# Kernel tuning notes

Measured on AMD Instinct MI355X. Metric: run time of the kernel, lower is better.

Reference implementation:

```python
import jax, jax.numpy as jnp
import numpy as np

THETA = 10000.0


def rope_apply(x, pos, theta=THETA):
    # x: [..., S, d] with d even; rotates interleaved pairs (2k, 2k+1),
    # matching the block-diag 2x2 rotation matmul in the torch RoPE.
    d = x.shape[-1]
    half = d // 2
    inv_freq = 1.0 / (theta ** (2.0 * jnp.arange(half, dtype=jnp.float32) / d))
    ang = pos.astype(jnp.float32)[:, None] * inv_freq[None, :]  # [S, half]
    cos, sin = jnp.cos(ang), jnp.sin(ang)
    xe, xo = x[..., 0::2], x[..., 1::2]
    oe = cos * xe - sin * xo
    oo = sin * xe + cos * xo
    return jnp.stack([oe, oo], axis=-1).reshape(x.shape)


def setup_inputs() -> dict:
    key = jax.random.key(0)
    ks = jax.random.split(key, 5)
    B, S, D = 2, 2048, 1024
    scale = 0.02
    return {
        "x": jax.random.normal(ks[0], (B, S, D), dtype=jnp.float32),
        "token_positions": jnp.arange(S, dtype=jnp.int64 if jax.config.jax_enable_x64 else jnp.int32),
        "wq": jax.random.normal(ks[1], (D, D), dtype=jnp.float32) * scale,
        "wk": jax.random.normal(ks[2], (D, D), dtype=jnp.float32) * scale,
        "wv": jax.random.normal(ks[3], (D, D), dtype=jnp.float32) * scale,
        "wo": jax.random.normal(ks[4], (D, D), dtype=jnp.float32) * scale,
    }


def reference(x, token_positions, wq, wk, wv, wo):
    B, S, D = x.shape
    H = 16
    dk = D // H

    def split_heads(t):  # [B,S,D] -> [B,H,S,dk]
        return t.reshape(B, S, H, dk).swapaxes(1, 2)

    q = split_heads(jnp.einsum('bsd,ed->bse', x, wq))
    k = split_heads(jnp.einsum('bsd,ed->bse', x, wk))
    v = split_heads(jnp.einsum('bsd,ed->bse', x, wv))

    q = rope_apply(q, token_positions)
    k = rope_apply(k, token_positions)

    scores = jnp.einsum('bhqd,bhkd->bhqk', q, k) / jnp.sqrt(jnp.float32(dk))
    causal = jnp.tril(jnp.ones((S, S), dtype=bool))
    scores = jnp.where(causal, scores, -jnp.inf)
    p = jax.nn.softmax(scores, axis=-1)
    o = jnp.einsum('bhqk,bhkd->bhqd', p, v)          # [B,H,S,dk]
    o = o.swapaxes(1, 2).reshape(B, S, D)            # merge heads
    return jnp.einsum('bse,de->bsd', o, wo)          # out proj (wo.T)
```

## Files before the change

### kernel.cpp

```cpp
#include <hip/hip_runtime.h>

typedef unsigned short u16;
typedef __attribute__((ext_vector_type(8))) short short8;
typedef __attribute__((ext_vector_type(4))) float f32x4;

__device__ __forceinline__ u16 f2b(float f) {
  union { float f; unsigned u; } v; v.f = f;
  unsigned u = v.u;
  return (u16)((u + 0x7FFFu + ((u >> 16) & 1u)) >> 16);
}
__device__ __forceinline__ u16 f2b_trunc(float f) {
  union { float f; unsigned u; } v; v.f = f;
  return (u16)(v.u >> 16);
}
__device__ __forceinline__ void glds16(const u16* g, u16* l) {
  __builtin_amdgcn_global_load_lds((const __attribute__((address_space(1))) void*)g,
                                   (__attribute__((address_space(3))) void*)l, 16, 0, 0);
}

__global__ __launch_bounds__(256) void prep_k(const float* __restrict__ x,
                                              const float* __restrict__ wq,
                                              const float* __restrict__ wk,
                                              const float* __restrict__ wv,
                                              const float* __restrict__ wo,
                                              const int* __restrict__ pos,
                                              u16* __restrict__ xb,
                                              u16* __restrict__ wqkvb,
                                              u16* __restrict__ wob,
                                              float* __restrict__ cs) {
  int bx = blockIdx.x, tid = threadIdx.x;
  if (bx < 8192) {
    const float* src; u16* dst; int base;
    if (bx < 4096)      { src = x;  dst = xb;                base = bx; }
    else if (bx < 5120) { src = wq; dst = wqkvb;             base = bx - 4096; }
    else if (bx < 6144) { src = wk; dst = wqkvb + (1 << 20); base = bx - 5120; }
    else if (bx < 7168) { src = wv; dst = wqkvb + (2 << 20); base = bx - 6144; }
    else                { src = wo; dst = wob;               base = bx - 7168; }
    int i4 = base * 1024 + tid * 4;
    const float4 v = *(const float4*)(src + i4);
    uint2 o;
    o.x = (unsigned)f2b(v.x) | ((unsigned)f2b(v.y) << 16);
    o.y = (unsigned)f2b(v.z) | ((unsigned)f2b(v.w) << 16);
    *(uint2*)(dst + i4) = o;
  } else {
    int idx = (bx - 8192) * 256 + tid;
    int i = idx & 31, s = idx >> 5;
    float p = (float)pos[s];
    float inv = expf(-(float)i * (logf(10000.0f) / 32.0f));
    float ang = p * inv;
    cs[idx * 2]     = cosf(ang);
    cs[idx * 2 + 1] = sinf(ang);
  }
}

__global__ __launch_bounds__(128, 3) void gemm_qkv(const u16* __restrict__ A,
                                                   const u16* __restrict__ B,
                                                   const float* __restrict__ cs,
                                                   u16* __restrict__ Qr,
                                                   u16* __restrict__ Kr,
                                                   u16* __restrict__ VTg) {
  const int K = 1024;
  __shared__ u16 As[64 * 64];
  __shared__ u16 Bs[128 * 64];
  const int tid = threadIdx.x;
  const int wv = tid >> 6, lane = tid & 63;
  const int quad = lane >> 4, l16 = lane & 15;
  const int m0 = blockIdx.y * 64, n0 = blockIdx.x * 128;
  const int sw = l16 & 7;

  f32x4 acc[4][4];
  for (int i = 0; i < 4; i++)
    for (int j = 0; j < 4; j++) acc[i][j] = (f32x4){0.f, 0.f, 0.f, 0.f};

  for (int kt = 0; kt < K; kt += 64) {
    __syncthreads();
#pragma unroll
    for (int p = 0; p < 4; p++) {
      int c = p * 128 + tid;
      int row = c >> 3, k8 = (c & 7) ^ (row & 7);
      glds16(A + (size_t)(m0 + row) * K + kt + k8 * 8, As + (size_t)(c & ~63) * 8);
    }
#pragma unroll
    for (int p = 0; p < 8; p++) {
      int c = p * 128 + tid;
      int row = c >> 3, k8 = (c & 7) ^ (row & 7);
      glds16(B + (size_t)(n0 + row) * K + kt + k8 * 8, Bs + (size_t)(c & ~63) * 8);
    }
    __syncthreads();
#pragma unroll
    for (int half = 0; half < 2; half++) {
      short8 af[4], bfr[4];
      const int kc = ((half * 4 + quad) ^ sw) * 8;
#pragma unroll
      for (int i = 0; i < 4; i++)
        af[i] = *(const short8*)(As + (i * 16 + l16) * 64 + kc);
#pragma unroll
      for (int j = 0; j < 4; j++)
        bfr[j] = *(const short8*)(Bs + (wv * 64 + j * 16 + l16) * 64 + kc);
#pragma unroll
      for (int i = 0; i < 4; i++)
#pragma unroll
        for (int j = 0; j < 4; j++)
          acc[i][j] = __builtin_amdgcn_mfma_f32_16x16x32_bf16(af[i], bfr[j], acc[i][j], 0, 0, 0);
    }
  }

  const int region = n0 >> 10;
  const int b = m0 >> 11;
  if (region < 2) {
    u16* dst = region ? Kr : Qr;
    const bool evn = (l16 & 1) == 0;
    for (int i = 0; i < 4; i++)
      for (int j = 0; j < 4; j++) {
        int col = n0 + wv * 64 + j * 16 + l16;
        int cq = col & 1023;
        int h = cq >> 6, d = cq & 63, ifr = (d >> 1) & 31;
        for (int r = 0; r < 4; r++) {
          int s = (m0 & 2047) + i * 16 + quad * 4 + r;
          float v = acc[i][j][r];
          float vp = __shfl_xor(v, 1);
          if (evn) {
            float2 c2 = *(const float2*)(cs + (s * 32 + ifr) * 2);
            float oe = c2.x * v - c2.y * vp;
            float oo = c2.y * v + c2.x * vp;
            unsigned pk = (unsigned)f2b(oe) | ((unsigned)f2b(oo) << 16);
            *(unsigned*)(dst + ((size_t)(b * 16 + h) * 2048 + s) * 64 + d) = pk;
          }
        }
      }
  } else {
    for (int j = 0; j < 4; j++) {
      int col = n0 + wv * 64 + j * 16 + l16;
      int cq = col & 1023;
      int h = cq >> 6, d = cq & 63;
      u16* base = VTg + ((size_t)(b * 16 + h) * 64 + d) * 2048;
      for (int i = 0; i < 4; i++) {
        int s0 = (m0 & 2047) + i * 16 + quad * 4;
        uint2 o;
        o.x = (unsigned)f2b(acc[i][j][0]) | ((unsigned)f2b(acc[i][j][1]) << 16);
        o.y = (unsigned)f2b(acc[i][j][2]) | ((unsigned)f2b(acc[i][j][3]) << 16);
        *(uint2*)(base + s0) = o;
      }
    }
  }
}

__global__ __launch_bounds__(128, 3) void gemm_bt_f32(const u16* __restrict__ A,
                                                      const u16* __restrict__ B,
                                                      float* __restrict__ C,
                                                      int M, int N, int K) {
  __shared__ u16 As[64 * 64];
  __shared__ u16 Bs[128 * 64];
  const int tid = threadIdx.x;
  const int wv = tid >> 6, lane = tid & 63;
  const int quad = lane >> 4, l16 = lane & 15;
  const int m0 = blockIdx.y * 64, n0 = blockIdx.x * 128;
  const int sw = l16 & 7;

  f32x4 acc[4][4];
  for (int i = 0; i < 4; i++)
    for (int j = 0; j < 4; j++) acc[i][j] = (f32x4){0.f, 0.f, 0.f, 0.f};

  for (int kt = 0; kt < K; kt += 64) {
    __syncthreads();
#pragma unroll
    for (int p = 0; p < 4; p++) {
      int c = p * 128 + tid;
      int row = c >> 3, k8 = (c & 7) ^ (row & 7);
      glds16(A + (size_t)(m0 + row) * K + kt + k8 * 8, As + (size_t)(c & ~63) * 8);
    }
#pragma unroll
    for (int p = 0; p < 8; p++) {
      int c = p * 128 + tid;
      int row = c >> 3, k8 = (c & 7) ^ (row & 7);
      glds16(B + (size_t)(n0 + row) * K + kt + k8 * 8, Bs + (size_t)(c & ~63) * 8);
    }
    __syncthreads();
#pragma unroll
    for (int half = 0; half < 2; half++) {
      short8 af[4], bfr[4];
      const int kc = ((half * 4 + quad) ^ sw) * 8;
#pragma unroll
      for (int i = 0; i < 4; i++)
        af[i] = *(const short8*)(As + (i * 16 + l16) * 64 + kc);
#pragma unroll
      for (int j = 0; j < 4; j++)
        bfr[j] = *(const short8*)(Bs + (wv * 64 + j * 16 + l16) * 64 + kc);
#pragma unroll
      for (int i = 0; i < 4; i++)
#pragma unroll
        for (int j = 0; j < 4; j++)
          acc[i][j] = __builtin_amdgcn_mfma_f32_16x16x32_bf16(af[i], bfr[j], acc[i][j], 0, 0, 0);
    }
  }
  for (int i = 0; i < 4; i++)
    for (int j = 0; j < 4; j++) {
      int col = n0 + wv * 64 + j * 16 + l16;
      for (int r = 0; r < 4; r++) {
        int row = m0 + i * 16 + quad * 4 + r;
        C[(size_t)row * N + col] = acc[i][j][r];
      }
    }
}

__global__ __launch_bounds__(256, 6) void attn_k(const u16* __restrict__ Q,
                                                 const u16* __restrict__ K,
                                                 const u16* __restrict__ VT,
                                                 u16* __restrict__ O, int S) {
  __shared__ u16 Ks[8 * 512], Vt[64 * 64], Ps[8 * 520];
  const int tid = threadIdx.x;
  const int wv = tid >> 6, lane = tid & 63, quad = lane >> 4, l16 = lane & 15;
  const int bh = blockIdx.x;
  const int yy = blockIdx.y, k4 = yy >> 3, g = yy & 7;
  const int qt = (k4 & 1) ? (k4 * 8 + 7 - g) : (k4 * 8 + g);
  const int q0 = qt * 64;
  const u16* Qg = Q + (size_t)bh * S * 64;
  const u16* Kg = K + (size_t)bh * S * 64;
  const u16* Vg = VT + (size_t)bh * S * 64;
  const float scale2 = 0.125f * 1.44269504f;
  const int rowbase = wv * 16 + quad * 4;

  const int vrow_off = lane >> 3;
  const int vchunk = (lane & 7) ^ (lane >> 3);

  const u16* qrow = Qg + (size_t)(q0 + wv * 16 + l16) * 64;
  short8 qa0 = *(const short8*)(qrow + quad * 8);
  short8 qa1 = *(const short8*)(qrow + 32 + quad * 8);

  f32x4 oacc[4];
  for (int j = 0; j < 4; j++) oacc[j] = (f32x4){0.f, 0.f, 0.f, 0.f};
  float l_r[4] = {0.f, 0.f, 0.f, 0.f};

  for (int kt = 0; kt <= qt; kt++) {
    const int k0 = kt * 64;
    __syncthreads();
    for (int p = wv; p < 8; p += 4) {
      glds16(Kg + (size_t)(k0 + lane) * 64 + p * 8, Ks + p * 512);
      glds16(Vg + (size_t)(p * 8 + vrow_off) * S + k0 + vchunk * 8, Vt + p * 512);
    }
    __syncthreads();

    const bool diag = (kt == qt);
#pragma unroll
    for (int nt = 0; nt < 4; nt++) {
      f32x4 s4 = (f32x4){0.f, 0.f, 0.f, 0.f};
      short8 b0 = *(const short8*)(Ks + quad * 512 + (nt * 16 + l16) * 8);
      short8 b1 = *(const short8*)(Ks + (4 + quad) * 512 + (nt * 16 + l16) * 8);
      s4 = __builtin_amdgcn_mfma_f32_16x16x32_bf16(qa0, b0, s4, 0, 0, 0);
      s4 = __builtin_amdgcn_mfma_f32_16x16x32_bf16(qa1, b1, s4, 0, 0, 0);
      int col = nt * 16 + l16;
      int cp = col >> 3, co = col & 7;
      if (!diag) {
#pragma unroll
        for (int r = 0; r < 4; r++) {
          float v = fminf(s4[r] * scale2, 86.f);
          float p = exp2f(v);
          l_r[r] += p;
          int row = rowbase + r;
          int A = (cp + 2 * (row >> 3)) & 7;
          Ps[A * 520 + row * 8 + co] = f2b_trunc(p);
        }
      } else {
#pragma unroll
        for (int r = 0; r < 4; r++) {
          float v = fminf(s4[r] * scale2, 86.f);
          if (col > rowbase + r) v = -1e30f;
          float p = exp2f(v);
          l_r[r] += p;
          int row = rowbase + r;
          int A = (cp + 2 * (row >> 3)) & 7;
          Ps[A * 520 + row * 8 + co] = f2b_trunc(p);
        }
      }
    }
    {
      int mr = wv * 16 + l16;
      int A0 = (quad + 2 * (mr >> 3)) & 7;
      short8 pa0 = *(const short8*)(Ps + A0 * 520 + mr * 8);
      short8 pa1 = *(const short8*)(Ps + ((A0 + 4) & 7) * 520 + mr * 8);
      int sl0 = quad ^ (l16 & 7);
#pragma unroll
      for (int nt = 0; nt < 4; nt++) {
        int d = nt * 16 + l16;
        short8 vb0 = *(const short8*)(Vt + d * 64 + sl0 * 8);
        short8 vb1 = *(const short8*)(Vt + d * 64 + (sl0 ^ 4) * 8);
        oacc[nt] = __builtin_amdgcn_mfma_f32_16x16x32_bf16(pa0, vb0, oacc[nt], 0, 0, 0);
        oacc[nt] = __builtin_amdgcn_mfma_f32_16x16x32_bf16(pa1, vb1, oacc[nt], 0, 0, 0);
      }
    }
  }
#pragma unroll
  for (int r = 0; r < 4; r++) {
    l_r[r] += __shfl_xor(l_r[r], 1);
    l_r[r] += __shfl_xor(l_r[r], 2);
    l_r[r] += __shfl_xor(l_r[r], 4);
    l_r[r] += __shfl_xor(l_r[r], 8);
    l_r[r] = 1.f / l_r[r];
  }
  const int b = bh >> 4, h = bh & 15;
  const bool evn = (l16 & 1) == 0;
#pragma unroll
  for (int nt = 0; nt < 4; nt++) {
    int col = nt * 16 + l16;
#pragma unroll
    for (int r = 0; r < 4; r++) {
      float v = oacc[nt][r] * l_r[r];
      float vp = __shfl_xor(v, 1);
      if (evn) {
        int s = q0 + rowbase + r;
        unsigned pk = (unsigned)f2b(v) | ((unsigned)f2b(vp) << 16);
        *(unsigned*)(O + ((size_t)(b * S + s) * 16 + h) * 64 + col) = pk;
      }
    }
  }
}

extern "C" void kernel_launch(void* const* d_in, const int* in_sizes, int n_in,
                              void* d_out, int out_size, void* d_ws, size_t ws_size,
                              hipStream_t stream) {
  const float* x  = (const float*)d_in[0];
  const int*   tp = (const int*)d_in[1];
  const float* wq = (const float*)d_in[2];
  const float* wk = (const float*)d_in[3];
  const float* wvp = (const float*)d_in[4];
  const float* wo = (const float*)d_in[5];
  float* out = (float*)d_out;

  const int S = 2048, D = 1024;
  const int BS = 2 * S;

  char* ws = (char*)d_ws;
  u16*   xb    = (u16*)(ws);
  u16*   wqkvb = (u16*)(ws + ((size_t)8 << 20));
  u16*   wob   = (u16*)(ws + ((size_t)14 << 20));
  float* cs    = (float*)(ws + ((size_t)16 << 20));
  u16*   qr    = (u16*)(ws + ((size_t)17 << 20));
  u16*   kr    = (u16*)(ws + ((size_t)25 << 20));
  u16*   vtg   = (u16*)(ws + ((size_t)33 << 20));
  u16*   ob    = (u16*)(ws + ((size_t)42 << 20));

  prep_k<<<8448, 256, 0, stream>>>(x, wq, wk, wvp, wo, tp, xb, wqkvb, wob, cs);

  dim3 g1(3 * D / 128, BS / 64);
  gemm_qkv<<<g1, 128, 0, stream>>>(xb, wqkvb, cs, qr, kr, vtg);

  dim3 ga(32, 32);
  attn_k<<<ga, 256, 0, stream>>>(qr, kr, vtg, ob, S);

  dim3 g2(D / 128, BS / 64);
  gemm_bt_f32<<<g2, 128, 0, stream>>>(ob, wob, out, BS, D, D);
}
```

Measured before the change: 205.1 us.

## Pair causal query tiles per block and double-buffer K/V loads

Each attention block now handles two query tiles, slot and 31-slot, so causal work is balanced across blocks and every K/V tile loaded into shared memory serves both tiles. K/V tiles are double-buffered so the load of the next tile overlaps compute on the current one, which removes one barrier per iteration. The grid is halved to 512 blocks and launch bounds drop from 6 to 2 blocks per CU. This raises register and LDS use and lowers occupancy.

```diff
diff --git a/kernel.cpp b/kernel.cpp
--- a/kernel.cpp
+++ b/kernel.cpp
@@ -203,113 +203,123 @@
     }
 }
 
-__global__ __launch_bounds__(256, 6) void attn_k(const u16* __restrict__ Q,
+__global__ __launch_bounds__(256, 2) void attn_k(const u16* __restrict__ Q,
                                                  const u16* __restrict__ K,
                                                  const u16* __restrict__ VT,
                                                  u16* __restrict__ O, int S) {
-  __shared__ u16 Ks[8 * 512], Vt[64 * 64], Ps[8 * 520];
+  __shared__ u16 Ks[2][8 * 512], Vt[2][8 * 512];
+  __shared__ u16 PsA[8 * 520], PsB[8 * 520];
   const int tid = threadIdx.x;
   const int wv = tid >> 6, lane = tid & 63, quad = lane >> 4, l16 = lane & 15;
-  const int bh = blockIdx.x;
-  const int yy = blockIdx.y, k4 = yy >> 3, g = yy & 7;
-  const int qt = (k4 & 1) ? (k4 * 8 + 7 - g) : (k4 * 8 + g);
-  const int q0 = qt * 64;
+  const int bh = blockIdx.x, slot = blockIdx.y;
+  const int qtA = slot, qtB = 31 - slot;
+  const int q0A = qtA * 64, q0B = qtB * 64;
   const u16* Qg = Q + (size_t)bh * S * 64;
   const u16* Kg = K + (size_t)bh * S * 64;
   const u16* Vg = VT + (size_t)bh * S * 64;
   const float scale2 = 0.125f * 1.44269504f;
   const int rowbase = wv * 16 + quad * 4;
-
   const int vrow_off = lane >> 3;
   const int vchunk = (lane & 7) ^ (lane >> 3);
 
-  const u16* qrow = Qg + (size_t)(q0 + wv * 16 + l16) * 64;
-  short8 qa0 = *(const short8*)(qrow + quad * 8);
-  short8 qa1 = *(const short8*)(qrow + 32 + quad * 8);
-
-  f32x4 oacc[4];
-  for (int j = 0; j < 4; j++) oacc[j] = (f32x4){0.f, 0.f, 0.f, 0.f};
-  float l_r[4] = {0.f, 0.f, 0.f, 0.f};
-
-  for (int kt = 0; kt <= qt; kt++) {
-    const int k0 = kt * 64;
-    __syncthreads();
-    for (int p = wv; p < 8; p += 4) {
-      glds16(Kg + (size_t)(k0 + lane) * 64 + p * 8, Ks + p * 512);
-      glds16(Vg + (size_t)(p * 8 + vrow_off) * S + k0 + vchunk * 8, Vt + p * 512);
-    }
-    __syncthreads();
-
-    const bool diag = (kt == qt);
+  const u16* qrowA = Qg + (size_t)(q0A + wv * 16 + l16) * 64;
+  short8 qa0A = *(const short8*)(qrowA + quad * 8);
+  short8 qa1A = *(const short8*)(qrowA + 32 + quad * 8);
+  const u16* qrowB = Qg + (size_t)(q0B + wv * 16 + l16) * 64;
+  short8 qa0B = *(const short8*)(qrowB + quad * 8);
+  short8 qa1B = *(const short8*)(qrowB + 32 + quad * 8);
+
+  f32x4 oaccA[4], oaccB[4];
+  for (int j = 0; j < 4; j++) {
+    oaccA[j] = (f32x4){0.f, 0.f, 0.f, 0.f};
+    oaccB[j] = (f32x4){0.f, 0.f, 0.f, 0.f};
+  }
+  float lA[4] = {0.f, 0.f, 0.f, 0.f}, lB[4] = {0.f, 0.f, 0.f, 0.f};
+
+  auto compute = [&](short8 qa0, short8 qa1, const u16* Ksb, const u16* Vtb,
+                     u16* Psb, f32x4* oacc, float* l_r, bool diag) {
 #pragma unroll
     for (int nt = 0; nt < 4; nt++) {
       f32x4 s4 = (f32x4){0.f, 0.f, 0.f, 0.f};
-      short8 b0 = *(const short8*)(Ks + quad * 512 + (nt * 16 + l16) * 8);
-      short8 b1 = *(const short8*)(Ks + (4 + quad) * 512 + (nt * 16 + l16) * 8);
+      short8 b0 = *(const short8*)(Ksb + quad * 512 + (nt * 16 + l16) * 8);
+      short8 b1 = *(const short8*)(Ksb + (4 + quad) * 512 + (nt * 16 + l16) * 8);
       s4 = __builtin_amdgcn_mfma_f32_16x16x32_bf16(qa0, b0, s4, 0, 0, 0);
       s4 = __builtin_amdgcn_mfma_f32_16x16x32_bf16(qa1, b1, s4, 0, 0, 0);
       int col = nt * 16 + l16;
       int cp = col >> 3, co = col & 7;
-      if (!diag) {
-#pragma unroll
-        for (int r = 0; r < 4; r++) {
-          float v = fminf(s4[r] * scale2, 86.f);
-          float p = exp2f(v);
-          l_r[r] += p;
-          int row = rowbase + r;
-          int A = (cp + 2 * (row >> 3)) & 7;
-          Ps[A * 520 + row * 8 + co] = f2b_trunc(p);
-        }
-      } else {
-#pragma unroll
-        for (int r = 0; r < 4; r++) {
-          float v = fminf(s4[r] * scale2, 86.f);
-          if (col > rowbase + r) v = -1e30f;
-          float p = exp2f(v);
-          l_r[r] += p;
-          int row = rowbase + r;
-          int A = (cp + 2 * (row >> 3)) & 7;
-          Ps[A * 520 + row * 8 + co] = f2b_trunc(p);
-        }
-      }
-    }
-    {
-      int mr = wv * 16 + l16;
-      int A0 = (quad + 2 * (mr >> 3)) & 7;
-      short8 pa0 = *(const short8*)(Ps + A0 * 520 + mr * 8);
-      short8 pa1 = *(const short8*)(Ps + ((A0 + 4) & 7) * 520 + mr * 8);
-      int sl0 = quad ^ (l16 & 7);
-#pragma unroll
-      for (int nt = 0; nt < 4; nt++) {
-        int d = nt * 16 + l16;
-        short8 vb0 = *(const short8*)(Vt + d * 64 + sl0 * 8);
-        short8 vb1 = *(const short8*)(Vt + d * 64 + (sl0 ^ 4) * 8);
-        oacc[nt] = __builtin_amdgcn_mfma_f32_16x16x32_bf16(pa0, vb0, oacc[nt], 0, 0, 0);
-        oacc[nt] = __builtin_amdgcn_mfma_f32_16x16x32_bf16(pa1, vb1, oacc[nt], 0, 0, 0);
-      }
-    }
-  }
-#pragma unroll
-  for (int r = 0; r < 4; r++) {
-    l_r[r] += __shfl_xor(l_r[r], 1);
-    l_r[r] += __shfl_xor(l_r[r], 2);
-    l_r[r] += __shfl_xor(l_r[r], 4);
-    l_r[r] += __shfl_xor(l_r[r], 8);
-    l_r[r] = 1.f / l_r[r];
-  }
+#pragma unroll
+      for (int r = 0; r < 4; r++) {
+        float v = fminf(s4[r] * scale2, 86.f);
+        if (diag && col > rowbase + r) v = -1e30f;
+        float p = exp2f(v);
+        l_r[r] += p;
+        int row = rowbase + r;
+        int A = (cp + 2 * (row >> 3)) & 7;
+        Psb[A * 520 + row * 8 + co] = f2b_trunc(p);
+      }
+    }
+    int mr = wv * 16 + l16;
+    int A0 = (quad + 2 * (mr >> 3)) & 7;
+    short8 pa0 = *(const short8*)(Psb + A0 * 520 + mr * 8);
+    short8 pa1 = *(const short8*)(Psb + ((A0 + 4) & 7) * 520 + mr * 8);
+    int sl0 = quad ^ (l16 & 7);
+#pragma unroll
+    for (int nt = 0; nt < 4; nt++) {
+      int d = nt * 16 + l16;
+      short8 vb0 = *(const short8*)(Vtb + d * 64 + sl0 * 8);
+      short8 vb1 = *(const short8*)(Vtb + d * 64 + (sl0 ^ 4) * 8);
+      oacc[nt] = __builtin_amdgcn_mfma_f32_16x16x32_bf16(pa0, vb0, oacc[nt], 0, 0, 0);
+      oacc[nt] = __builtin_amdgcn_mfma_f32_16x16x32_bf16(pa1, vb1, oacc[nt], 0, 0, 0);
+    }
+  };
+
+  for (int p = wv; p < 8; p += 4) {
+    glds16(Kg + (size_t)(lane)*64 + p * 8, &Ks[0][p * 512]);
+    glds16(Vg + (size_t)(p * 8 + vrow_off) * S + vchunk * 8, &Vt[0][p * 512]);
+  }
+
+  for (int kt = 0; kt <= qtB; kt++) {
+    const int cur = kt & 1;
+    __syncthreads();
+    if (kt < qtB) {
+      const int kn = (kt + 1) * 64;
+      for (int p = wv; p < 8; p += 4) {
+        glds16(Kg + (size_t)(kn + lane) * 64 + p * 8, &Ks[cur ^ 1][p * 512]);
+        glds16(Vg + (size_t)(p * 8 + vrow_off) * S + kn + vchunk * 8, &Vt[cur ^ 1][p * 512]);
+      }
+    }
+    compute(qa0B, qa1B, &Ks[cur][0], &Vt[cur][0], PsB, oaccB, lB, kt == qtB);
+    if (kt <= qtA)
+      compute(qa0A, qa1A, &Ks[cur][0], &Vt[cur][0], PsA, oaccA, lA, kt == qtA);
+  }
+
   const int b = bh >> 4, h = bh & 15;
   const bool evn = (l16 & 1) == 0;
 #pragma unroll
+  for (int r = 0; r < 4; r++) {
+    lA[r] += __shfl_xor(lA[r], 1); lA[r] += __shfl_xor(lA[r], 2);
+    lA[r] += __shfl_xor(lA[r], 4); lA[r] += __shfl_xor(lA[r], 8);
+    lA[r] = 1.f / lA[r];
+    lB[r] += __shfl_xor(lB[r], 1); lB[r] += __shfl_xor(lB[r], 2);
+    lB[r] += __shfl_xor(lB[r], 4); lB[r] += __shfl_xor(lB[r], 8);
+    lB[r] = 1.f / lB[r];
+  }
+#pragma unroll
   for (int nt = 0; nt < 4; nt++) {
     int col = nt * 16 + l16;
 #pragma unroll
     for (int r = 0; r < 4; r++) {
-      float v = oacc[nt][r] * l_r[r];
-      float vp = __shfl_xor(v, 1);
+      float vA = oaccA[nt][r] * lA[r];
+      float vAp = __shfl_xor(vA, 1);
+      float vB = oaccB[nt][r] * lB[r];
+      float vBp = __shfl_xor(vB, 1);
       if (evn) {
-        int s = q0 + rowbase + r;
-        unsigned pk = (unsigned)f2b(v) | ((unsigned)f2b(vp) << 16);
-        *(unsigned*)(O + ((size_t)(b * S + s) * 16 + h) * 64 + col) = pk;
+        int sA = q0A + rowbase + r;
+        unsigned pkA = (unsigned)f2b(vA) | ((unsigned)f2b(vAp) << 16);
+        *(unsigned*)(O + ((size_t)(b * S + sA) * 16 + h) * 64 + col) = pkA;
+        int sB = q0B + rowbase + r;
+        unsigned pkB = (unsigned)f2b(vB) | ((unsigned)f2b(vBp) << 16);
+        *(unsigned*)(O + ((size_t)(b * S + sB) * 16 + h) * 64 + col) = pkB;
       }
     }
   }
@@ -344,7 +354,7 @@
   dim3 g1(3 * D / 128, BS / 64);
   gemm_qkv<<<g1, 128, 0, stream>>>(xb, wqkvb, cs, qr, kr, vtg);
 
-  dim3 ga(32, 32);
+  dim3 ga(32, 16);
   attn_k<<<ga, 256, 0, stream>>>(qr, kr, vtg, ob, S);
 
   dim3 g2(D / 128, BS / 64);
```

New measurement: 198.0 us. 1.04x faster.

## Pair complementary causal query tiles per block, double-buffer K/V, prescale Q

Applied to the files above, without the earlier changes.

Each attention block now has 512 threads in two wave groups. One group handles query tile `slot` and the other handles tile 31-slot, so every block does the same amount of causal work while sharing the K/V tiles it stages. K/V loads into LDS are double-buffered so the next tile's global-to-LDS copy is issued before the current tile is computed. The softmax scale and log2e factor are folded into Q in the QKV GEMM epilogue, which removes a multiply and the clamp from the inner loop; dropping the fminf clamp slightly changes overflow safety. The grid halves and LDS use per block grows, which changes occupancy.

```diff
diff --git a/kernel.cpp b/kernel.cpp
--- a/kernel.cpp
+++ b/kernel.cpp
@@ -109,6 +109,7 @@
   const int b = m0 >> 11;
   if (region < 2) {
     u16* dst = region ? Kr : Qr;
+    const float qs = region ? 1.0f : 0.125f * 1.44269504f;
     const bool evn = (l16 & 1) == 0;
     for (int i = 0; i < 4; i++)
       for (int j = 0; j < 4; j++) {
@@ -121,8 +122,8 @@
           float vp = __shfl_xor(v, 1);
           if (evn) {
             float2 c2 = *(const float2*)(cs + (s * 32 + ifr) * 2);
-            float oe = c2.x * v - c2.y * vp;
-            float oo = c2.y * v + c2.x * vp;
+            float oe = (c2.x * v - c2.y * vp) * qs;
+            float oo = (c2.y * v + c2.x * vp) * qs;
             unsigned pk = (unsigned)f2b(oe) | ((unsigned)f2b(oo) << 16);
             *(unsigned*)(dst + ((size_t)(b * 16 + h) * 2048 + s) * 64 + d) = pk;
           }
@@ -203,102 +204,105 @@
     }
 }
 
-__global__ __launch_bounds__(256, 6) void attn_k(const u16* __restrict__ Q,
+struct AttnSM {
+  u16 Ks[2][8 * 512];
+  u16 Vt[2][8 * 512];
+  u16 Ps[2][8 * 520];
+};
+
+template <bool DIAG>
+__device__ __forceinline__ void attn_tile(const u16* Ksb, const u16* Vtb, u16* Psb,
+                                          short8 qa0, short8 qa1, f32x4* oacc,
+                                          float* l_r, int wl, int quad, int l16) {
+  const int rowbase = wl * 16 + quad * 4;
+#pragma unroll
+  for (int nt = 0; nt < 4; nt++) {
+    f32x4 s4 = (f32x4){0.f, 0.f, 0.f, 0.f};
+    short8 b0 = *(const short8*)(Ksb + quad * 512 + (nt * 16 + l16) * 8);
+    short8 b1 = *(const short8*)(Ksb + (4 + quad) * 512 + (nt * 16 + l16) * 8);
+    s4 = __builtin_amdgcn_mfma_f32_16x16x32_bf16(qa0, b0, s4, 0, 0, 0);
+    s4 = __builtin_amdgcn_mfma_f32_16x16x32_bf16(qa1, b1, s4, 0, 0, 0);
+    int col = nt * 16 + l16;
+    int cp = col >> 3, co = col & 7;
+#pragma unroll
+    for (int r = 0; r < 4; r++) {
+      float v = s4[r];
+      if (DIAG && col > rowbase + r) v = -1e30f;
+      float p = exp2f(v);
+      l_r[r] += p;
+      int row = rowbase + r;
+      int A = (cp + 2 * (row >> 3)) & 7;
+      Psb[A * 520 + row * 8 + co] = f2b_trunc(p);
+    }
+  }
+  int mr = wl * 16 + l16;
+  int A0 = (quad + 2 * (mr >> 3)) & 7;
+  short8 pa0 = *(const short8*)(Psb + A0 * 520 + mr * 8);
+  short8 pa1 = *(const short8*)(Psb + ((A0 + 4) & 7) * 520 + mr * 8);
+  int sl0 = quad ^ (l16 & 7);
+#pragma unroll
+  for (int nt = 0; nt < 4; nt++) {
+    int d = nt * 16 + l16;
+    short8 vb0 = *(const short8*)(Vtb + d * 64 + sl0 * 8);
+    short8 vb1 = *(const short8*)(Vtb + d * 64 + (sl0 ^ 4) * 8);
+    oacc[nt] = __builtin_amdgcn_mfma_f32_16x16x32_bf16(pa0, vb0, oacc[nt], 0, 0, 0);
+    oacc[nt] = __builtin_amdgcn_mfma_f32_16x16x32_bf16(pa1, vb1, oacc[nt], 0, 0, 0);
+  }
+}
+
+__global__ __launch_bounds__(512, 4) void attn_k(const u16* __restrict__ Q,
                                                  const u16* __restrict__ K,
                                                  const u16* __restrict__ VT,
                                                  u16* __restrict__ O, int S) {
-  __shared__ u16 Ks[8 * 512], Vt[64 * 64], Ps[8 * 520];
+  __shared__ AttnSM sm;
   const int tid = threadIdx.x;
   const int wv = tid >> 6, lane = tid & 63, quad = lane >> 4, l16 = lane & 15;
-  const int bh = blockIdx.x;
-  const int yy = blockIdx.y, k4 = yy >> 3, g = yy & 7;
-  const int qt = (k4 & 1) ? (k4 * 8 + 7 - g) : (k4 * 8 + g);
-  const int q0 = qt * 64;
+  const int grp = wv >> 2, wl = wv & 3;
+  const int bh = blockIdx.x, slot = blockIdx.y;
+  const int qtB = 31 - slot;
+  const int qtMy = grp ? qtB : slot;
+  const int q0My = qtMy * 64;
   const u16* Qg = Q + (size_t)bh * S * 64;
   const u16* Kg = K + (size_t)bh * S * 64;
   const u16* Vg = VT + (size_t)bh * S * 64;
-  const float scale2 = 0.125f * 1.44269504f;
-  const int rowbase = wv * 16 + quad * 4;
-
   const int vrow_off = lane >> 3;
   const int vchunk = (lane & 7) ^ (lane >> 3);
 
-  const u16* qrow = Qg + (size_t)(q0 + wv * 16 + l16) * 64;
+  const u16* qrow = Qg + (size_t)(q0My + wl * 16 + l16) * 64;
   short8 qa0 = *(const short8*)(qrow + quad * 8);
   short8 qa1 = *(const short8*)(qrow + 32 + quad * 8);
 
   f32x4 oacc[4];
   for (int j = 0; j < 4; j++) oacc[j] = (f32x4){0.f, 0.f, 0.f, 0.f};
   float l_r[4] = {0.f, 0.f, 0.f, 0.f};
-
-  for (int kt = 0; kt <= qt; kt++) {
-    const int k0 = kt * 64;
-    __syncthreads();
-    for (int p = wv; p < 8; p += 4) {
-      glds16(Kg + (size_t)(k0 + lane) * 64 + p * 8, Ks + p * 512);
-      glds16(Vg + (size_t)(p * 8 + vrow_off) * S + k0 + vchunk * 8, Vt + p * 512);
-    }
-    __syncthreads();
-
-    const bool diag = (kt == qt);
-#pragma unroll
-    for (int nt = 0; nt < 4; nt++) {
-      f32x4 s4 = (f32x4){0.f, 0.f, 0.f, 0.f};
-      short8 b0 = *(const short8*)(Ks + quad * 512 + (nt * 16 + l16) * 8);
-      short8 b1 = *(const short8*)(Ks + (4 + quad) * 512 + (nt * 16 + l16) * 8);
-      s4 = __builtin_amdgcn_mfma_f32_16x16x32_bf16(qa0, b0, s4, 0, 0, 0);
-      s4 = __builtin_amdgcn_mfma_f32_16x16x32_bf16(qa1, b1, s4, 0, 0, 0);
-      int col = nt * 16 + l16;
-      int cp = col >> 3, co = col & 7;
-      if (!diag) {
-#pragma unroll
-        for (int r = 0; r < 4; r++) {
-          float v = fminf(s4[r] * scale2, 86.f);
-          float p = exp2f(v);
-          l_r[r] += p;
-          int row = rowbase + r;
-          int A = (cp + 2 * (row >> 3)) & 7;
-          Ps[A * 520 + row * 8 + co] = f2b_trunc(p);
-        }
-      } else {
-#pragma unroll
-        for (int r = 0; r < 4; r++) {
-          float v = fminf(s4[r] * scale2, 86.f);
-          if (col > rowbase + r) v = -1e30f;
-          float p = exp2f(v);
-          l_r[r] += p;
-          int row = rowbase + r;
-          int A = (cp + 2 * (row >> 3)) & 7;
-          Ps[A * 520 + row * 8 + co] = f2b_trunc(p);
-        }
-      }
-    }
-    {
-      int mr = wv * 16 + l16;
-      int A0 = (quad + 2 * (mr >> 3)) & 7;
-      short8 pa0 = *(const short8*)(Ps + A0 * 520 + mr * 8);
-      short8 pa1 = *(const short8*)(Ps + ((A0 + 4) & 7) * 520 + mr * 8);
-      int sl0 = quad ^ (l16 & 7);
-#pragma unroll
-      for (int nt = 0; nt < 4; nt++) {
-        int d = nt * 16 + l16;
-        short8 vb0 = *(const short8*)(Vt + d * 64 + sl0 * 8);
-        short8 vb1 = *(const short8*)(Vt + d * 64 + (sl0 ^ 4) * 8);
-        oacc[nt] = __builtin_amdgcn_mfma_f32_16x16x32_bf16(pa0, vb0, oacc[nt], 0, 0, 0);
-        oacc[nt] = __builtin_amdgcn_mfma_f32_16x16x32_bf16(pa1, vb1, oacc[nt], 0, 0, 0);
-      }
-    }
-  }
-#pragma unroll
-  for (int r = 0; r < 4; r++) {
-    l_r[r] += __shfl_xor(l_r[r], 1);
-    l_r[r] += __shfl_xor(l_r[r], 2);
-    l_r[r] += __shfl_xor(l_r[r], 4);
-    l_r[r] += __shfl_xor(l_r[r], 8);
-    l_r[r] = 1.f / l_r[r];
-  }
+  u16* Psb = &sm.Ps[grp][0];
+
+  glds16(Kg + (size_t)lane * 64 + wv * 8, &sm.Ks[0][wv * 512]);
+  glds16(Vg + (size_t)(wv * 8 + vrow_off) * S + vchunk * 8, &sm.Vt[0][wv * 512]);
+
+  for (int kt = 0; kt <= qtB; kt++) {
+    const int cur = kt & 1;
+    __syncthreads();
+    if (kt < qtB) {
+      const int kn = (kt + 1) * 64;
+      glds16(Kg + (size_t)(kn + lane) * 64 + wv * 8, &sm.Ks[cur ^ 1][wv * 512]);
+      glds16(Vg + (size_t)(wv * 8 + vrow_off) * S + kn + vchunk * 8, &sm.Vt[cur ^ 1][wv * 512]);
+    }
+    if (kt < qtMy)
+      attn_tile<false>(&sm.Ks[cur][0], &sm.Vt[cur][0], Psb, qa0, qa1, oacc, l_r, wl, quad, l16);
+    else if (kt == qtMy)
+      attn_tile<true>(&sm.Ks[cur][0], &sm.Vt[cur][0], Psb, qa0, qa1, oacc, l_r, wl, quad, l16);
+  }
+
   const int b = bh >> 4, h = bh & 15;
   const bool evn = (l16 & 1) == 0;
+  const int rowbase = wl * 16 + quad * 4;
+#pragma unroll
+  for (int r = 0; r < 4; r++) {
+    l_r[r] += __shfl_xor(l_r[r], 1); l_r[r] += __shfl_xor(l_r[r], 2);
+    l_r[r] += __shfl_xor(l_r[r], 4); l_r[r] += __shfl_xor(l_r[r], 8);
+    l_r[r] = 1.f / l_r[r];
+  }
 #pragma unroll
   for (int nt = 0; nt < 4; nt++) {
     int col = nt * 16 + l16;
@@ -307,7 +311,7 @@
       float v = oacc[nt][r] * l_r[r];
       float vp = __shfl_xor(v, 1);
       if (evn) {
-        int s = q0 + rowbase + r;
+        int s = q0My + rowbase + r;
         unsigned pk = (unsigned)f2b(v) | ((unsigned)f2b(vp) << 16);
         *(unsigned*)(O + ((size_t)(b * S + s) * 16 + h) * 64 + col) = pk;
       }
@@ -344,8 +348,8 @@
   dim3 g1(3 * D / 128, BS / 64);
   gemm_qkv<<<g1, 128, 0, stream>>>(xb, wqkvb, cs, qr, kr, vtg);
 
-  dim3 ga(32, 32);
-  attn_k<<<ga, 256, 0, stream>>>(qr, kr, vtg, ob, S);
+  dim3 ga(32, 16);
+  attn_k<<<ga, 512, 0, stream>>>(qr, kr, vtg, ob, S);
 
   dim3 g2(D / 128, BS / 64);
   gemm_bt_f32<<<g2, 128, 0, stream>>>(ob, wob, out, BS, D, D);
```

Result: faster. 186.5 us (-9.0%).
